# Kernel tuning notes

Hardware: AMD Instinct MI355X
Metric: run time of the kernel (lower is better)

The kernel has to match this reference:

```python
import jax, jax.numpy as jnp
import numpy as np

NEG_SLOPE = 0.01  # torch LeakyReLU default
MIN_FREQ = 1.0
MAX_FREQ = 10.0
W = 100
N_HIDDEN = 100
N_OBS = 64

def _leaky(x):
    return jnp.where(x >= 0, x, NEG_SLOPE * x)

def setup_inputs() -> dict:
    key = jax.random.key(0)
    ks = jax.random.split(key, 7)
    # kaiming_uniform-ish init scales (exact init doesn't matter for correctness baseline)
    def unif(k, shape, fan_in):
        bound = np.sqrt(6.0 / fan_in)
        return jax.random.uniform(k, shape, jnp.float32, -bound, bound)
    x = jax.random.normal(ks[0], (65536, N_OBS), jnp.float32)
    W_in = unif(ks[1], (N_OBS, W), N_OBS)
    b_in = jnp.zeros((W,), jnp.float32)
    Ws = unif(ks[2], (N_HIDDEN, W, W), W)
    bs = jnp.zeros((N_HIDDEN, W), jnp.float32)
    W_out = unif(ks[3], (W, 1), W)
    b_out = jnp.zeros((1,), jnp.float32)
    return {"x": x, "W_in": W_in, "b_in": b_in, "Ws": Ws, "bs": bs,
            "W_out": W_out, "b_out": b_out}

def reference(x, W_in, b_in, Ws, bs, W_out, b_out):
    h = _leaky(x @ W_in + b_in)                       # [B, 100]
    def layer(h, wb):
        w, b = wb
        return _leaky(h @ w + b), None
    h, _ = jax.lax.scan(layer, h, (Ws, bs))           # 100 hidden layers
    a = h @ W_out + b_out                             # [B, 1]
    a = jnp.tanh(a)
    return (a + 1.0) / 2.0 * (MAX_FREQ - MIN_FREQ) + MIN_FREQ
```

## Files before the change

### kernel.cpp

```cpp
#include <hip/hip_runtime.h>
#include <cmath>

#define NLAYERS 100
#define DIN     64
#define WDIM    100
#define NTT     4
#define RT      2
#define ROWS    64
#define KS      7
#define PSTR    136
#define BUF     (64 * PSTR)

typedef _Float16 half8  __attribute__((ext_vector_type(8)));
typedef _Float16 half2v __attribute__((ext_vector_type(2)));
typedef __fp16   fp16x2 __attribute__((ext_vector_type(2)));
typedef float    f32x4  __attribute__((ext_vector_type(4)));
typedef float    f32x16 __attribute__((ext_vector_type(16)));

#define WSH_LAYER_HALVES (KS * NTT * 64 * 8)
#define WSH_HALVES       (NLAYERS * WSH_LAYER_HALVES)
#define W0_HALVES        (4 * NTT * 64 * 8)
#define BPAD_FLOATS      128
#define OFF_BPAD_B       ((WSH_HALVES + W0_HALVES) * 2)
#define OFF_WOUT_B       (OFF_BPAD_B + BPAD_FLOATS * 4)
#define WOUT_FLOATS      128

__global__ __launch_bounds__(256)
void actor_prep(const float* __restrict__ Win, const float* __restrict__ bin,
                const float* __restrict__ Ws,  const float* __restrict__ bs,
                const float* __restrict__ Wout,
                _Float16* __restrict__ wsh, _Float16* __restrict__ w0sh,
                float* __restrict__ bpad, float* __restrict__ woutp) {
    __shared__ float tile[16 * 128];
    const int bid = blockIdx.x, tid = threadIdx.x;
    if (bid < NLAYERS * KS) {
        const int l = bid / KS, ks = bid % KS;
#pragma unroll
        for (int e = 0; e < 8; ++e) {
            int idx = tid + 256 * e;
            int kk = idx >> 7, nn = idx & 127;
            int k = ks * 16 + kk;
            float v = 0.f;
            if (k < WDIM && nn < WDIM)        v = Ws[(l * WDIM + k) * WDIM + nn];
            else if (k == WDIM && nn < WDIM)  v = bs[l * WDIM + nn];
            else if (k == WDIM && nn == WDIM) v = 1.0f;
            tile[idx] = v;
        }
        __syncthreads();
        const int lane = tid & 63, nt = tid >> 6;
        const int g = lane >> 5, n = nt * 32 + (lane & 31);
        half8 o;
#pragma unroll
        for (int j = 0; j < 8; ++j) o[j] = (_Float16)tile[(g * 8 + j) * 128 + n];
        *(half8*)(wsh + (((l * KS + ks) * NTT + nt) << 9) + lane * 8) = o;
        return;
    }
    int b2 = bid - NLAYERS * KS;
    if (b2 < 4) {
        const int ks = b2;
#pragma unroll
        for (int e = 0; e < 8; ++e) {
            int idx = tid + 256 * e;
            int kk = idx >> 7, nn = idx & 127;
            int k = ks * 16 + kk;
            tile[idx] = (nn < WDIM) ? Win[k * WDIM + nn] : 0.f;
        }
        __syncthreads();
        const int lane = tid & 63, nt = tid >> 6;
        const int g = lane >> 5, n = nt * 32 + (lane & 31);
        half8 o;
#pragma unroll
        for (int j = 0; j < 8; ++j) o[j] = (_Float16)tile[(g * 8 + j) * 128 + n];
        *(half8*)(w0sh + ((ks * NTT + nt) << 9) + lane * 8) = o;
        return;
    }
    if (tid < BPAD_FLOATS) {
        bpad[tid] = (tid < WDIM) ? bin[tid] : (tid == WDIM ? 1.0f : 0.f);
    } else {
        int t = tid - BPAD_FLOATS;
        if (t < WOUT_FLOATS) woutp[t] = (t < WDIM) ? Wout[t] : 0.f;
    }
}

__device__ __forceinline__ void split8(const float* __restrict__ p, half8& hi, half8& lo) {
    f32x4 u0 = *(const f32x4*)p;
    f32x4 u1 = *(const f32x4*)(p + 4);
    float v[8] = {u0[0], u0[1], u0[2], u0[3], u1[0], u1[1], u1[2], u1[3]};
#pragma unroll
    for (int e = 0; e < 8; e += 2) {
        fp16x2 h = __builtin_amdgcn_cvt_pkrtz(v[e], v[e + 1]);
        float r0 = v[e]     - (float)h[0];
        float r1 = v[e + 1] - (float)h[1];
        fp16x2 l = __builtin_amdgcn_cvt_pkrtz(r0, r1);
        hi[e] = (_Float16)h[0]; hi[e + 1] = (_Float16)h[1];
        lo[e] = (_Float16)l[0]; lo[e + 1] = (_Float16)l[1];
    }
}

__device__ __forceinline__ void ep_quad(const f32x16 a, int qd, _Float16* __restrict__ d) {
    half2v p01, p23;
    p01[0] = (_Float16)a[4 * qd + 0]; p01[1] = (_Float16)a[4 * qd + 1];
    p23[0] = (_Float16)a[4 * qd + 2]; p23[1] = (_Float16)a[4 * qd + 3];
    const half2v slope = {(_Float16)0.01f, (_Float16)0.01f};
    p01 = __builtin_elementwise_max(p01, p01 * slope);
    p23 = __builtin_elementwise_max(p23, p23 * slope);
    uint2 w;
    w.x = __builtin_bit_cast(unsigned, p01);
    w.y = __builtin_bit_cast(unsigned, p23);
    *reinterpret_cast<uint2*>(d) = w;
}

__global__ __launch_bounds__(256, 4)
void actor_main(const float* __restrict__ x,
                const _Float16* __restrict__ wsh,
                const _Float16* __restrict__ w0sh,
                const float* __restrict__ bpad,
                const float* __restrict__ woutp,
                const float* __restrict__ bout,
                float* __restrict__ out) {
    __shared__ __align__(16) _Float16 hp[2 * BUF];
    const int lane = threadIdx.x & 63;
    const int wid  = threadIdx.x >> 6;
    const int g = lane >> 5, b31 = lane & 31;
    const int sw = ((b31 >> 3) & 1) << 5;
    const int rowbase = blockIdx.x * ROWS;

    f32x16 acc[RT];
    half8 wb[KS];
    const f32x16 zero16 = {0,0,0,0, 0,0,0,0, 0,0,0,0, 0,0,0,0};

    {
        half8 w0[4];
#pragma unroll
        for (int ks = 0; ks < 4; ++ks)
            w0[ks] = *(const half8*)(w0sh + (ks * NTT + wid) * 512 + lane * 8);
#pragma unroll
        for (int rt = 0; rt < RT; ++rt)
#pragma unroll
            for (int qd = 0; qd < 4; ++qd) {
                f32x4 tq = *(const f32x4*)(bpad + wid * 32 + 8 * qd + 4 * g);
#pragma unroll
                for (int r = 0; r < 4; ++r) acc[rt][4 * qd + r] = tq[r];
            }
#pragma unroll
        for (int rt = 0; rt < RT; ++rt) {
            const float* xr = x + (rowbase + rt * 32 + b31) * DIN;
#pragma unroll
            for (int ks = 0; ks < 4; ++ks) {
                half8 xhi, xlo;
                split8(xr + ks * 16 + g * 8, xhi, xlo);
                acc[rt] = __builtin_amdgcn_mfma_f32_32x32x16_f16(w0[ks], xhi, acc[rt], 0, 0, 0);
                acc[rt] = __builtin_amdgcn_mfma_f32_32x32x16_f16(w0[ks], xlo, acc[rt], 0, 0, 0);
            }
        }
    }
#pragma unroll
    for (int rt = 0; rt < RT; ++rt) {
        _Float16* d = hp + (rt * 32 + b31) * PSTR + ((wid * 32 + 4 * g) ^ sw);
#pragma unroll
        for (int qd = 0; qd < 4; ++qd) ep_quad(acc[rt], qd, d + 8 * qd);
    }
#pragma unroll
    for (int ks = 0; ks < KS; ++ks)
        wb[ks] = *(const half8*)(wsh + (ks * NTT + wid) * 512 + lane * 8);
    asm volatile("s_waitcnt lgkmcnt(0)\n\ts_barrier" ::: "memory");

#pragma unroll 1
    for (int l = 0; l < NLAYERS; ++l) {
        const _Float16* rb = hp + (l & 1) * BUF;
        _Float16* wbf = hp + ((l + 1) & 1) * BUF;
        const _Float16* wn = wsh + (l < NLAYERS - 1 ? l + 1 : l) * WSH_LAYER_HALVES;
        half8 bh[KS];

#pragma unroll
        for (int ks = 0; ks < KS; ++ks)
            bh[ks] = *(const half8*)(rb + b31 * PSTR + ((ks * 16 + g * 8) ^ sw));
#pragma unroll
        for (int ks = 0; ks < KS; ++ks)
            acc[0] = __builtin_amdgcn_mfma_f32_32x32x16_f16(
                wb[ks], bh[ks], (ks == 0 ? zero16 : acc[0]), 0, 0, 0);

#pragma unroll
        for (int ks = 0; ks < KS; ++ks)
            bh[ks] = *(const half8*)(rb + (32 + b31) * PSTR + ((ks * 16 + g * 8) ^ sw));
        _Float16* d0 = wbf + b31 * PSTR + ((wid * 32 + 4 * g) ^ sw);
#pragma unroll
        for (int ks = 0; ks < KS; ++ks) {
            acc[1] = __builtin_amdgcn_mfma_f32_32x32x16_f16(
                wb[ks], bh[ks], (ks == 0 ? zero16 : acc[1]), 0, 0, 0);
            wb[ks] = *(const half8*)(wn + (ks * NTT + wid) * 512 + lane * 8);
            if (ks < 4)
                ep_quad(acc[0], ks, d0 + 8 * ks);
        }
        {
            _Float16* d1 = wbf + (32 + b31) * PSTR + ((wid * 32 + 4 * g) ^ sw);
#pragma unroll
            for (int qd = 0; qd < 4; ++qd) ep_quad(acc[1], qd, d1 + 8 * qd);
        }
        asm volatile("s_waitcnt lgkmcnt(0)\n\ts_barrier" ::: "memory");
    }

    float part[RT];
#pragma unroll
    for (int rt = 0; rt < RT; ++rt) {
        float s = 0.f;
#pragma unroll
        for (int qd = 0; qd < 4; ++qd) {
            f32x4 w4 = *(const f32x4*)(woutp + wid * 32 + 8 * qd + 4 * g);
#pragma unroll
            for (int r = 0; r < 4; ++r) {
                float a = acc[rt][4 * qd + r];
                float v = fmaxf(a, 0.01f * a);
                s += v * w4[r];
            }
        }
        s += __shfl_xor(s, 32);
        part[rt] = s;
    }
    float* red = (float*)hp;
    if (lane < 32) {
        red[wid * 64 + b31]      = part[0];
        red[wid * 64 + 32 + b31] = part[1];
    }
    __syncthreads();
    {
        const int r = threadIdx.x;
        if (r < 64) {
            float tot = red[r] + red[64 + r] + red[128 + r] + red[192 + r] + bout[0];
            out[rowbase + r] = tanhf(tot) * 4.5f + 5.5f;
        }
    }
}

extern "C" void kernel_launch(void* const* d_in, const int* in_sizes, int n_in,
                              void* d_out, int out_size, void* d_ws, size_t ws_size,
                              hipStream_t stream) {
    const float* x    = (const float*)d_in[0];
    const float* Win  = (const float*)d_in[1];
    const float* bin  = (const float*)d_in[2];
    const float* Ws   = (const float*)d_in[3];
    const float* bs   = (const float*)d_in[4];
    const float* Wout = (const float*)d_in[5];
    const float* bout = (const float*)d_in[6];
    float* out = (float*)d_out;

    char* ws = (char*)d_ws;
    _Float16* wsh  = (_Float16*)ws;
    _Float16* w0sh = wsh + WSH_HALVES;
    float* bpad  = (float*)(ws + OFF_BPAD_B);
    float* woutp = (float*)(ws + OFF_WOUT_B);

    hipLaunchKernelGGL(actor_prep, dim3(NLAYERS * KS + 4 + 1), dim3(256), 0, stream,
                       Win, bin, Ws, bs, Wout, wsh, w0sh, bpad, woutp);

    const int nrows = in_sizes[0] / DIN;
    hipLaunchKernelGGL(actor_main, dim3(nrows / ROWS), dim3(256), 0, stream,
                       x, wsh, w0sh, bpad, woutp, bout, out);
}
```

Baseline: 276.3 us.

## Retile main kernel to 32-row blocks with two N-tiles per wave

Measured after the change: 302.8 us. 9.6% more time.

```diff
diff --git a/kernel.cpp b/kernel.cpp
--- a/kernel.cpp
+++ b/kernel.cpp
@@ -5,11 +5,11 @@
 #define DIN     64
 #define WDIM    100
 #define NTT     4
-#define RT      2
-#define ROWS    64
+#define NTW     2
+#define ROWS    32
 #define KS      7
 #define PSTR    136
-#define BUF     (64 * PSTR)
+#define BUF     (ROWS * PSTR)
 
 typedef _Float16 half8  __attribute__((ext_vector_type(8)));
 typedef _Float16 half2v __attribute__((ext_vector_type(2)));
@@ -110,7 +110,7 @@
     *reinterpret_cast<uint2*>(d) = w;
 }
 
-__global__ __launch_bounds__(256, 4)
+__global__ __launch_bounds__(128, 4)
 void actor_main(const float* __restrict__ x,
                 const _Float16* __restrict__ wsh,
                 const _Float16* __restrict__ w0sh,
@@ -124,45 +124,50 @@
     const int g = lane >> 5, b31 = lane & 31;
     const int sw = ((b31 >> 3) & 1) << 5;
     const int rowbase = blockIdx.x * ROWS;
-
-    f32x16 acc[RT];
-    half8 wb[KS];
+    const int ntb = wid * NTW;
+
+    f32x16 acc[NTW];
+    half8 wb[KS][NTW];
     const f32x16 zero16 = {0,0,0,0, 0,0,0,0, 0,0,0,0, 0,0,0,0};
 
     {
-        half8 w0[4];
+        half8 w0[4][NTW];
 #pragma unroll
         for (int ks = 0; ks < 4; ++ks)
-            w0[ks] = *(const half8*)(w0sh + (ks * NTT + wid) * 512 + lane * 8);
-#pragma unroll
-        for (int rt = 0; rt < RT; ++rt)
+#pragma unroll
+            for (int ntl = 0; ntl < NTW; ++ntl)
+                w0[ks][ntl] = *(const half8*)(w0sh + (ks * NTT + ntb + ntl) * 512 + lane * 8);
+#pragma unroll
+        for (int ntl = 0; ntl < NTW; ++ntl)
 #pragma unroll
             for (int qd = 0; qd < 4; ++qd) {
-                f32x4 tq = *(const f32x4*)(bpad + wid * 32 + 8 * qd + 4 * g);
-#pragma unroll
-                for (int r = 0; r < 4; ++r) acc[rt][4 * qd + r] = tq[r];
-            }
-#pragma unroll
-        for (int rt = 0; rt < RT; ++rt) {
-            const float* xr = x + (rowbase + rt * 32 + b31) * DIN;
-#pragma unroll
-            for (int ks = 0; ks < 4; ++ks) {
-                half8 xhi, xlo;
-                split8(xr + ks * 16 + g * 8, xhi, xlo);
-                acc[rt] = __builtin_amdgcn_mfma_f32_32x32x16_f16(w0[ks], xhi, acc[rt], 0, 0, 0);
-                acc[rt] = __builtin_amdgcn_mfma_f32_32x32x16_f16(w0[ks], xlo, acc[rt], 0, 0, 0);
-            }
-        }
-    }
-#pragma unroll
-    for (int rt = 0; rt < RT; ++rt) {
-        _Float16* d = hp + (rt * 32 + b31) * PSTR + ((wid * 32 + 4 * g) ^ sw);
-#pragma unroll
-        for (int qd = 0; qd < 4; ++qd) ep_quad(acc[rt], qd, d + 8 * qd);
+                f32x4 tq = *(const f32x4*)(bpad + (ntb + ntl) * 32 + 8 * qd + 4 * g);
+#pragma unroll
+                for (int r = 0; r < 4; ++r) acc[ntl][4 * qd + r] = tq[r];
+            }
+        const float* xr = x + (rowbase + b31) * DIN;
+#pragma unroll
+        for (int ks = 0; ks < 4; ++ks) {
+            half8 xhi, xlo;
+            split8(xr + ks * 16 + g * 8, xhi, xlo);
+#pragma unroll
+            for (int ntl = 0; ntl < NTW; ++ntl) {
+                acc[ntl] = __builtin_amdgcn_mfma_f32_32x32x16_f16(w0[ks][ntl], xhi, acc[ntl], 0, 0, 0);
+                acc[ntl] = __builtin_amdgcn_mfma_f32_32x32x16_f16(w0[ks][ntl], xlo, acc[ntl], 0, 0, 0);
+            }
+        }
+    }
+#pragma unroll
+    for (int ntl = 0; ntl < NTW; ++ntl) {
+        _Float16* d = hp + b31 * PSTR + (((ntb + ntl) * 32 + 4 * g) ^ sw);
+#pragma unroll
+        for (int qd = 0; qd < 4; ++qd) ep_quad(acc[ntl], qd, d + 8 * qd);
     }
 #pragma unroll
     for (int ks = 0; ks < KS; ++ks)
-        wb[ks] = *(const half8*)(wsh + (ks * NTT + wid) * 512 + lane * 8);
+#pragma unroll
+        for (int ntl = 0; ntl < NTW; ++ntl)
+            wb[ks][ntl] = *(const half8*)(wsh + (ks * NTT + ntb + ntl) * 512 + lane * 8);
     asm volatile("s_waitcnt lgkmcnt(0)\n\ts_barrier" ::: "memory");
 
 #pragma unroll 1
@@ -176,59 +181,47 @@
         for (int ks = 0; ks < KS; ++ks)
             bh[ks] = *(const half8*)(rb + b31 * PSTR + ((ks * 16 + g * 8) ^ sw));
 #pragma unroll
-        for (int ks = 0; ks < KS; ++ks)
+        for (int ks = 0; ks < KS; ++ks) {
             acc[0] = __builtin_amdgcn_mfma_f32_32x32x16_f16(
-                wb[ks], bh[ks], (ks == 0 ? zero16 : acc[0]), 0, 0, 0);
-
-#pragma unroll
-        for (int ks = 0; ks < KS; ++ks)
-            bh[ks] = *(const half8*)(rb + (32 + b31) * PSTR + ((ks * 16 + g * 8) ^ sw));
-        _Float16* d0 = wbf + b31 * PSTR + ((wid * 32 + 4 * g) ^ sw);
-#pragma unroll
-        for (int ks = 0; ks < KS; ++ks) {
+                wb[ks][0], bh[ks], (ks == 0 ? zero16 : acc[0]), 0, 0, 0);
             acc[1] = __builtin_amdgcn_mfma_f32_32x32x16_f16(
-                wb[ks], bh[ks], (ks == 0 ? zero16 : acc[1]), 0, 0, 0);
-            wb[ks] = *(const half8*)(wn + (ks * NTT + wid) * 512 + lane * 8);
-            if (ks < 4)
-                ep_quad(acc[0], ks, d0 + 8 * ks);
+                wb[ks][1], bh[ks], (ks == 0 ? zero16 : acc[1]), 0, 0, 0);
+            wb[ks][0] = *(const half8*)(wn + (ks * NTT + ntb + 0) * 512 + lane * 8);
+            wb[ks][1] = *(const half8*)(wn + (ks * NTT + ntb + 1) * 512 + lane * 8);
         }
         {
-            _Float16* d1 = wbf + (32 + b31) * PSTR + ((wid * 32 + 4 * g) ^ sw);
-#pragma unroll
-            for (int qd = 0; qd < 4; ++qd) ep_quad(acc[1], qd, d1 + 8 * qd);
+            _Float16* d0 = wbf + b31 * PSTR + (((ntb + 0) * 32 + 4 * g) ^ sw);
+            _Float16* d1 = wbf + b31 * PSTR + (((ntb + 1) * 32 + 4 * g) ^ sw);
+#pragma unroll
+            for (int qd = 0; qd < 4; ++qd) {
+                ep_quad(acc[0], qd, d0 + 8 * qd);
+                ep_quad(acc[1], qd, d1 + 8 * qd);
+            }
         }
         asm volatile("s_waitcnt lgkmcnt(0)\n\ts_barrier" ::: "memory");
     }
 
-    float part[RT];
-#pragma unroll
-    for (int rt = 0; rt < RT; ++rt) {
-        float s = 0.f;
+    float s = 0.f;
+#pragma unroll
+    for (int ntl = 0; ntl < NTW; ++ntl)
 #pragma unroll
         for (int qd = 0; qd < 4; ++qd) {
-            f32x4 w4 = *(const f32x4*)(woutp + wid * 32 + 8 * qd + 4 * g);
+            f32x4 w4 = *(const f32x4*)(woutp + (ntb + ntl) * 32 + 8 * qd + 4 * g);
 #pragma unroll
             for (int r = 0; r < 4; ++r) {
-                float a = acc[rt][4 * qd + r];
+                float a = acc[ntl][4 * qd + r];
                 float v = fmaxf(a, 0.01f * a);
                 s += v * w4[r];
             }
         }
-        s += __shfl_xor(s, 32);
-        part[rt] = s;
-    }
+    s += __shfl_xor(s, 32);
     float* red = (float*)hp;
-    if (lane < 32) {
-        red[wid * 64 + b31]      = part[0];
-        red[wid * 64 + 32 + b31] = part[1];
-    }
+    if (lane < 32) red[wid * 32 + b31] = s;
     __syncthreads();
-    {
+    if (threadIdx.x < 32) {
         const int r = threadIdx.x;
-        if (r < 64) {
-            float tot = red[r] + red[64 + r] + red[128 + r] + red[192 + r] + bout[0];
-            out[rowbase + r] = tanhf(tot) * 4.5f + 5.5f;
-        }
+        float tot = red[r] + red[32 + r] + bout[0];
+        out[rowbase + r] = tanhf(tot) * 4.5f + 5.5f;
     }
 }
 
@@ -254,6 +247,6 @@
                        Win, bin, Ws, bs, Wout, wsh, w0sh, bpad, woutp);
 
     const int nrows = in_sizes[0] / DIN;
-    hipLaunchKernelGGL(actor_main, dim3(nrows / ROWS), dim3(256), 0, stream,
+    hipLaunchKernelGGL(actor_main, dim3(nrows / ROWS), dim3(128), 0, stream,
                        x, wsh, w0sh, bpad, woutp, bout, out);
 }
```
